# Kernel optimization log

Hardware: AMD Instinct MI355X
Metric: run time of the kernel (lower is better)

The kernel has to match this reference:

```python
import jax, jax.numpy as jnp
import numpy as np

BS, S, D, H, DFF, L = 8, 1024, 256, 8, 1024, 3
DK = D // H
NEG = -1e32


def setup_inputs() -> dict:
    key = jax.random.key(0)
    ks = jax.random.split(key, 10)
    r = lambda k, shp: jax.random.normal(k, shp, jnp.float32) * 0.02
    return {
        "q_embed_data": jax.random.normal(ks[0], (BS, S, D), jnp.float32),
        "qa_embed_data": jax.random.normal(ks[1], (BS, S, D), jnp.float32),
        "Wk": r(ks[2], (L, D, D)), "bk": jnp.zeros((L, D), jnp.float32),
        "Wv": r(ks[3], (L, D, D)), "bv": jnp.zeros((L, D), jnp.float32),
        "Wo": r(ks[4], (L, D, D)), "bo": jnp.zeros((L, D), jnp.float32),
        "gammas": r(ks[5], (L, H)),
        "ln1_g": jnp.ones((L, D), jnp.float32), "ln1_b": jnp.zeros((L, D), jnp.float32),
        "W1": r(ks[6], (L, D, DFF)), "b1": jnp.zeros((L, DFF), jnp.float32),
        "W2": r(ks[7], (L, DFF, D)), "b2": jnp.zeros((L, D), jnp.float32),
        "ln2_g": jnp.ones((L, D), jnp.float32), "ln2_b": jnp.zeros((L, D), jnp.float32),
    }


def _layernorm(x, g, b, eps=1e-5):
    mu = x.mean(-1, keepdims=True)
    var = ((x - mu) ** 2).mean(-1, keepdims=True)
    return (x - mu) * jax.lax.rsqrt(var + eps) * g + b


def _attn(xq, xk, xv, Wk, bk, Wv, bv, Wo, bo, gamma, mask, zero_pad):
    # kq_same=1: q and k both use k_linear
    bs = xq.shape[0]
    q = (xq @ Wk + bk).reshape(bs, S, H, DK).transpose(0, 2, 1, 3)  # bhsd
    k = (xk @ Wk + bk).reshape(bs, S, H, DK).transpose(0, 2, 1, 3)
    v = (xv @ Wv + bv).reshape(bs, S, H, DK).transpose(0, 2, 1, 3)
    scores = jnp.einsum('bhid,bhjd->bhij', q, k) / np.float32(np.sqrt(DK))
    mf = mask.astype(scores.dtype)
    # no-grad decay branch (detached in torch)
    p = jax.nn.softmax(jnp.where(mask, scores, NEG), axis=-1) * mf
    distcum = jnp.cumsum(p, axis=-1)
    disttot = p.sum(axis=-1, keepdims=True)
    idx = jnp.arange(S)
    pos = jnp.abs(idx[None, :] - idx[:, None]).astype(jnp.float32)[None, None]
    dist = jnp.sqrt(jnp.clip((disttot - distcum) * pos, 0.0, None))
    dist = jax.lax.stop_gradient(dist)
    g = -jax.nn.softplus(gamma)[None, :, None, None]  # (1,H,1,1)
    total_effect = jnp.clip(jnp.exp(dist * g), 1e-5, 1e5)
    scores = scores * total_effect
    attn = jax.nn.softmax(jnp.where(mask, scores, NEG), axis=-1)
    if zero_pad:
        attn = attn.at[:, :, 0, :].set(0.0)
    out = jnp.einsum('bhij,bhjd->bhid', attn, v)
    out = out.transpose(0, 2, 1, 3).reshape(bs, S, D)
    return out @ Wo + bo


def _block(i, xq, xk, xv, mask, zero_pad, apply_pos, P):
    Wk, bk, Wv, bv, Wo, bo, gam, l1g, l1b, W1, b1, W2, b2, l2g, l2b = [p[i] for p in P]
    q2 = _attn(xq, xk, xv, Wk, bk, Wv, bv, Wo, bo, gam, mask, zero_pad)
    x = _layernorm(xq + q2, l1g, l1b)
    if apply_pos:
        ff = jax.nn.relu(x @ W1 + b1) @ W2 + b2
        x = _layernorm(x + ff, l2g, l2b)
    return x


def _forward(q_embed_data, qa_embed_data, Wk, bk, Wv, bv, Wo, bo, gammas,
             ln1_g, ln1_b, W1, b1, W2, b2, ln2_g, ln2_b):
    P = (Wk, bk, Wv, bv, Wo, bo, gammas, ln1_g, ln1_b, W1, b1, W2, b2, ln2_g, ln2_b)
    tri_incl = jnp.tril(jnp.ones((S, S), bool))[None, None]       # mask=1: peek current+past
    tri_excl = jnp.tril(jnp.ones((S, S), bool), -1)[None, None]   # mask=0: strictly past
    x, y = q_embed_data, qa_embed_data
    # blocks_1 (n_blocks=1): mask=1, apply_pos=True, self-attn on y
    y = _block(0, y, y, y, tri_incl, False, True, P)
    # blocks_2 (2*n_blocks=2): alternate (mask=1, no FFN) / (mask=0, zero_pad, FFN, values=y)
    x = _block(1, x, x, x, tri_incl, False, False, P)
    x = _block(2, x, x, y, tri_excl, True, True, P)
    return x


def reference(q_embed_data, qa_embed_data, Wk, bk, Wv, bv, Wo, bo, gammas,
              ln1_g, ln1_b, W1, b1, W2, b2, ln2_g, ln2_b):
    return _forward(q_embed_data, qa_embed_data, Wk, bk, Wv, bv, Wo, bo, gammas,
                    ln1_g, ln1_b, W1, b1, W2, b2, ln2_g, ln2_b)
```

## Files before the change

### kernel.cpp

```cpp
#include <hip/hip_runtime.h>

typedef unsigned short u16;
typedef float f32x4 __attribute__((ext_vector_type(4)));
typedef __bf16 bf16x8 __attribute__((ext_vector_type(8)));
typedef u16 u16x8 __attribute__((ext_vector_type(8)));
typedef u16 u16x4 __attribute__((ext_vector_type(4)));

__device__ __forceinline__ u16 f2bf(float f) {
  union { float f; unsigned u; } v; v.f = f;
  unsigned r = (v.u + 0x7FFFu + ((v.u >> 16) & 1u)) >> 16;
  return (u16)r;
}
__device__ __forceinline__ unsigned cvtpk_bf16(float lo, float hi) {
  unsigned r;
  asm("v_cvt_pk_bf16_f32 %0, %1, %2" : "=v"(r) : "v"(lo), "v"(hi));
  return r;
}

__global__ __launch_bounds__(256) void gemm_vt_kernel(
    const u16* __restrict__ A, const u16* __restrict__ Bt,
    const float* __restrict__ bias, u16* __restrict__ vT, int M, int N, int K) {
  __shared__ u16 As[64 * 64];
  __shared__ u16 Bs[64 * 64];
  const int tid = threadIdx.x;
  const int lane = tid & 63;
  const int w = tid >> 6;
  const int m0 = blockIdx.x * 64;
  const int n0 = blockIdx.y * 64;
  const int wr = (w >> 1) * 32;
  const int wc = (w & 1) * 32;
  const int l15 = lane & 15, hi = lane >> 4;

  f32x4 acc[2][2] = {};

  for (int k0 = 0; k0 < K; k0 += 64) {
#pragma unroll
    for (int rep = 0; rep < 2; ++rep) {
      int idx = tid + rep * 256;
      int row = idx >> 3, c8 = idx & 7;
      int cs = ((c8 ^ (row & 7)) << 3);
      __builtin_amdgcn_global_load_lds(
          (const __attribute__((address_space(1))) void*)(A + (size_t)(m0 + row) * K + k0 + cs),
          (__attribute__((address_space(3))) void*)(&As[idx * 8]), 16, 0, 0);
      __builtin_amdgcn_global_load_lds(
          (const __attribute__((address_space(1))) void*)(Bt + (size_t)(n0 + row) * K + k0 + cs),
          (__attribute__((address_space(3))) void*)(&Bs[idx * 8]), 16, 0, 0);
    }
    __syncthreads();
#pragma unroll
    for (int kk = 0; kk < 2; ++kk) {
      int kb = (kk * 32 + (hi << 3)) << 1;
      bf16x8 af[2], bfr[2];
#pragma unroll
      for (int mf = 0; mf < 2; ++mf) {
        int m = wr + mf * 16 + l15;
        af[mf] = *(const bf16x8*)((const char*)As + m * 128 + (kb ^ ((m & 7) << 4)));
      }
#pragma unroll
      for (int nf = 0; nf < 2; ++nf) {
        int n = wc + nf * 16 + l15;
        bfr[nf] = *(const bf16x8*)((const char*)Bs + n * 128 + (kb ^ ((n & 7) << 4)));
      }
#pragma unroll
      for (int mf = 0; mf < 2; ++mf)
#pragma unroll
        for (int nf = 0; nf < 2; ++nf)
          acc[mf][nf] = __builtin_amdgcn_mfma_f32_16x16x32_bf16(af[mf], bfr[nf], acc[mf][nf], 0, 0, 0);
    }
    __syncthreads();
  }

#pragma unroll
  for (int mf = 0; mf < 2; ++mf)
#pragma unroll
    for (int nf = 0; nf < 2; ++nf) {
      int col = n0 + wc + nf * 16 + l15;
      float bia = bias[col];
      u16x4 tv;
#pragma unroll
      for (int r = 0; r < 4; ++r) {
        float val = acc[mf][nf][r] + bia;
        tv[r] = f2bf(val);
      }
      int row0 = m0 + wr + mf * 16 + (hi << 2);
      size_t addr = (((size_t)(row0 >> 10) * 8 + (col >> 5)) * 32 + (col & 31)) * 1024 + (row0 & 1023);
      *(u16x4*)(vT + addr) = tv;
    }
}

template <int RELU>
__global__ __launch_bounds__(256) void gemm_w_kernel(
    const u16* __restrict__ A, const u16* __restrict__ Bt,
    const float* __restrict__ bias, u16* __restrict__ Cbf,
    int M, int N, int K) {
  __shared__ u16 As[64 * 64];
  __shared__ u16 Bs[128 * 64];
  const int tid = threadIdx.x;
  const int lane = tid & 63;
  const int w = tid >> 6;
  const int m0 = blockIdx.x * 64;
  const int n0 = blockIdx.y * 128;
  const int wr = (w >> 1) * 32;
  const int wc = (w & 1) * 64;
  const int l15 = lane & 15, hi = lane >> 4;

  f32x4 acc[2][4] = {};

  for (int k0 = 0; k0 < K; k0 += 64) {
#pragma unroll
    for (int rep = 0; rep < 2; ++rep) {
      int idx = tid + rep * 256;
      int row = idx >> 3, c8 = idx & 7;
      int cs = ((c8 ^ (row & 7)) << 3);
      __builtin_amdgcn_global_load_lds(
          (const __attribute__((address_space(1))) void*)(A + (size_t)(m0 + row) * K + k0 + cs),
          (__attribute__((address_space(3))) void*)(&As[idx * 8]), 16, 0, 0);
    }
#pragma unroll
    for (int rep = 0; rep < 4; ++rep) {
      int idx = tid + rep * 256;
      int row = idx >> 3, c8 = idx & 7;
      int cs = ((c8 ^ (row & 7)) << 3);
      __builtin_amdgcn_global_load_lds(
          (const __attribute__((address_space(1))) void*)(Bt + (size_t)(n0 + row) * K + k0 + cs),
          (__attribute__((address_space(3))) void*)(&Bs[idx * 8]), 16, 0, 0);
    }
    __syncthreads();
#pragma unroll
    for (int kk = 0; kk < 2; ++kk) {
      int kb = (kk * 32 + (hi << 3)) << 1;
      bf16x8 af[2], bfr[4];
#pragma unroll
      for (int mf = 0; mf < 2; ++mf) {
        int m = wr + mf * 16 + l15;
        af[mf] = *(const bf16x8*)((const char*)As + m * 128 + (kb ^ ((m & 7) << 4)));
      }
#pragma unroll
      for (int nf = 0; nf < 4; ++nf) {
        int n = wc + nf * 16 + l15;
        bfr[nf] = *(const bf16x8*)((const char*)Bs + n * 128 + (kb ^ ((n & 7) << 4)));
      }
#pragma unroll
      for (int mf = 0; mf < 2; ++mf)
#pragma unroll
        for (int nf = 0; nf < 4; ++nf)
          acc[mf][nf] = __builtin_amdgcn_mfma_f32_16x16x32_bf16(af[mf], bfr[nf], acc[mf][nf], 0, 0, 0);
    }
    __syncthreads();
  }

#pragma unroll
  for (int mf = 0; mf < 2; ++mf)
#pragma unroll
    for (int nf = 0; nf < 4; ++nf) {
      int col = n0 + wc + nf * 16 + l15;
      float bia = bias[col];
#pragma unroll
      for (int r = 0; r < 4; ++r) {
        int row = m0 + wr + mf * 16 + (hi << 2) + r;
        float val = acc[mf][nf][r] + bia;
        if (RELU) val = fmaxf(val, 0.f);
        Cbf[(size_t)row * N + col] = f2bf(val);
      }
    }
}

__global__ __launch_bounds__(256) void gemm_kv_kernel(
    const u16* __restrict__ A, const u16* __restrict__ Bt,
    const float* __restrict__ biasK, const float* __restrict__ biasV,
    u16* __restrict__ qkbf, u16* __restrict__ vT, int M, int N, int K) {
  __shared__ u16 As[64 * 64];
  __shared__ u16 Bs[128 * 64];
  const int tid = threadIdx.x;
  const int lane = tid & 63;
  const int w = tid >> 6;
  const int m0 = blockIdx.x * 64;
  const int n0 = blockIdx.y * 128;
  const int wr = (w >> 1) * 32;
  const int wc = (w & 1) * 64;
  const int l15 = lane & 15, hi = lane >> 4;

  f32x4 acc[2][4] = {};

  for (int k0 = 0; k0 < K; k0 += 64) {
#pragma unroll
    for (int rep = 0; rep < 2; ++rep) {
      int idx = tid + rep * 256;
      int row = idx >> 3, c8 = idx & 7;
      int cs = ((c8 ^ (row & 7)) << 3);
      __builtin_amdgcn_global_load_lds(
          (const __attribute__((address_space(1))) void*)(A + (size_t)(m0 + row) * K + k0 + cs),
          (__attribute__((address_space(3))) void*)(&As[idx * 8]), 16, 0, 0);
    }
#pragma unroll
    for (int rep = 0; rep < 4; ++rep) {
      int idx = tid + rep * 256;
      int row = idx >> 3, c8 = idx & 7;
      int cs = ((c8 ^ (row & 7)) << 3);
      __builtin_amdgcn_global_load_lds(
          (const __attribute__((address_space(1))) void*)(Bt + (size_t)(n0 + row) * K + k0 + cs),
          (__attribute__((address_space(3))) void*)(&Bs[idx * 8]), 16, 0, 0);
    }
    __syncthreads();
#pragma unroll
    for (int kk = 0; kk < 2; ++kk) {
      int kb = (kk * 32 + (hi << 3)) << 1;
      bf16x8 af[2], bfr[4];
#pragma unroll
      for (int mf = 0; mf < 2; ++mf) {
        int m = wr + mf * 16 + l15;
        af[mf] = *(const bf16x8*)((const char*)As + m * 128 + (kb ^ ((m & 7) << 4)));
      }
#pragma unroll
      for (int nf = 0; nf < 4; ++nf) {
        int n = wc + nf * 16 + l15;
        bfr[nf] = *(const bf16x8*)((const char*)Bs + n * 128 + (kb ^ ((n & 7) << 4)));
      }
#pragma unroll
      for (int mf = 0; mf < 2; ++mf)
#pragma unroll
        for (int nf = 0; nf < 4; ++nf)
          acc[mf][nf] = __builtin_amdgcn_mfma_f32_16x16x32_bf16(af[mf], bfr[nf], acc[mf][nf], 0, 0, 0);
    }
    __syncthreads();
  }

#pragma unroll
  for (int mf = 0; mf < 2; ++mf)
#pragma unroll
    for (int nf = 0; nf < 4; ++nf) {
      int col = n0 + wc + nf * 16 + l15;
      const bool isV = (col >= 256);
      float bia = isV ? biasV[col - 256] : biasK[col];
      u16x4 tv;
#pragma unroll
      for (int r = 0; r < 4; ++r) {
        int row = m0 + wr + mf * 16 + (hi << 2) + r;
        float val = acc[mf][nf][r] + bia;
        if (!isV) qkbf[(size_t)row * 256 + col] = f2bf(val);
        tv[r] = f2bf(val);
      }
      if (isV) {
        int row0 = m0 + wr + mf * 16 + (hi << 2);
        int vc = col - 256;
        size_t addr = (((size_t)(row0 >> 10) * 8 + (vc >> 5)) * 32 + (vc & 31)) * 1024 + (row0 & 1023);
        *(u16x4*)(vT + addr) = tv;
      }
    }
}

__global__ __launch_bounds__(256) void gemm_ln_kernel(
    const u16* __restrict__ A, const u16* __restrict__ Bt,
    const float* __restrict__ bias, const float* __restrict__ res,
    const float* __restrict__ g, const float* __restrict__ b,
    float* __restrict__ outf, u16* __restrict__ outb, int K) {
  __shared__ u16 As[32 * 64];
  __shared__ u16 Bs[256 * 64];
  __shared__ float red[2][32][2];

  const int tid = threadIdx.x;
  const int lane = tid & 63;
  const int w = tid >> 6;
  const int rowgrp = w >> 1, colh = w & 1;
  const int m0 = blockIdx.x * 32;
  const int l15 = lane & 15, hi = lane >> 4;

  f32x4 acc[8] = {};

  for (int k0 = 0; k0 < K; k0 += 64) {
    {
      int row = tid >> 3, c8 = tid & 7;
      int cs = ((c8 ^ (row & 7)) << 3);
      __builtin_amdgcn_global_load_lds(
          (const __attribute__((address_space(1))) void*)(A + (size_t)(m0 + row) * K + k0 + cs),
          (__attribute__((address_space(3))) void*)(&As[tid * 8]), 16, 0, 0);
    }
#pragma unroll
    for (int rep = 0; rep < 8; ++rep) {
      int idx = tid + rep * 256;
      int row = idx >> 3, c8 = idx & 7;
      int cs = ((c8 ^ (row & 7)) << 3);
      __builtin_amdgcn_global_load_lds(
          (const __attribute__((address_space(1))) void*)(Bt + (size_t)row * K + k0 + cs),
          (__attribute__((address_space(3))) void*)(&Bs[idx * 8]), 16, 0, 0);
    }
    __syncthreads();
#pragma unroll
    for (int kk = 0; kk < 2; ++kk) {
      int kb = (kk * 32 + (hi << 3)) << 1;
      int m = rowgrp * 16 + l15;
      bf16x8 af = *(const bf16x8*)((const char*)As + m * 128 + (kb ^ ((m & 7) << 4)));
      bf16x8 bfr[8];
#pragma unroll
      for (int nf = 0; nf < 8; ++nf) {
        int n = colh * 128 + nf * 16 + l15;
        bfr[nf] = *(const bf16x8*)((const char*)Bs + n * 128 + (kb ^ ((n & 7) << 4)));
      }
#pragma unroll
      for (int nf = 0; nf < 8; ++nf)
        acc[nf] = __builtin_amdgcn_mfma_f32_16x16x32_bf16(af, bfr[nf], acc[nf], 0, 0, 0);
    }
    __syncthreads();
  }

  const int rbase = m0 + rowgrp * 16 + hi * 4;
  float s[4] = {0.f, 0.f, 0.f, 0.f}, ss[4] = {0.f, 0.f, 0.f, 0.f};
#pragma unroll
  for (int nf = 0; nf < 8; ++nf) {
    int col = colh * 128 + nf * 16 + l15;
    float bia = bias[col];
#pragma unroll
    for (int r = 0; r < 4; ++r) {
      float v = acc[nf][r] + bia + res[(size_t)(rbase + r) * 256 + col];
      acc[nf][r] = v;
      s[r] += v;
      ss[r] += v * v;
    }
  }
#pragma unroll
  for (int r = 0; r < 4; ++r) {
#pragma unroll
    for (int o = 1; o < 16; o <<= 1) {
      s[r] += __shfl_xor(s[r], o);
      ss[r] += __shfl_xor(ss[r], o);
    }
  }
  if (l15 == 0) {
#pragma unroll
    for (int r = 0; r < 4; ++r) {
      red[colh][rowgrp * 16 + hi * 4 + r][0] = s[r];
      red[colh][rowgrp * 16 + hi * 4 + r][1] = ss[r];
    }
  }
  __syncthreads();
  float mu[4], rs[4];
#pragma unroll
  for (int r = 0; r < 4; ++r) {
    int rr = rowgrp * 16 + hi * 4 + r;
    float S = red[0][rr][0] + red[1][rr][0];
    float SS = red[0][rr][1] + red[1][rr][1];
    mu[r] = S * (1.f / 256.f);
    float var = SS * (1.f / 256.f) - mu[r] * mu[r];
    rs[r] = rsqrtf(var + 1e-5f);
  }
#pragma unroll
  for (int nf = 0; nf < 8; ++nf) {
    int col = colh * 128 + nf * 16 + l15;
    float gv = g[col], bv = b[col];
#pragma unroll
    for (int r = 0; r < 4; ++r) {
      float o = (acc[nf][r] - mu[r]) * rs[r] * gv + bv;
      size_t addr = (size_t)(rbase + r) * 256 + col;
      outf[addr] = o;
      outb[addr] = f2bf(o);
    }
  }
}

__global__ __launch_bounds__(256) void attn_mfma_kernel(
    const u16* __restrict__ qkbf, const u16* __restrict__ vT,
    u16* __restrict__ ao, const float* __restrict__ gam, int excl) {
  __shared__ float zbuf[4][16];
  __shared__ float z2buf[4][16];
  __shared__ float accbuf[8][4][64];

  const int lane = threadIdx.x & 63, w = threadIdx.x >> 6;
  const int qt = 63 - blockIdx.y;
  const int bh = blockIdx.x;
  const int b = bh >> 3, h = bh & 7;
  const int q0 = qt * 16;
  const int l15 = lane & 15, hi = lane >> 4;
  const int i = q0 + l15;
  const float LOG2E = 1.4426950408889634f;
  const float g2 = -log1pf(__expf(gam[h])) * LOG2E;
  const float cscale = 0.17677669529663687f * LOG2E;
  const float CLIP2 = -16.609640474436812f;

  const u16* kbase = qkbf + (size_t)b * 1024 * 256 + h * 32;
  const u16* vbase = vT + (size_t)bh * 32 * 1024;
  const bf16x8 qfrag = *(const bf16x8*)(kbase + (size_t)i * 256 + hi * 8);

  const int mylim = i - excl;
  const int jmax = q0 + 15 - excl;
  const int ntiles = (jmax >> 4) + 1;
  const int C = (ntiles + 3) >> 2;
  const int c0 = w * C;
  const int tEnd = (c0 + C < ntiles) ? (c0 + C) : ntiles;
  const int count = (tEnd > c0) ? (tEnd - c0) : 0;

  auto calc_l = [&](int t, float* l) {
    bf16x8 kf = *(const bf16x8*)(kbase + (size_t)(t * 16 + l15) * 256 + hi * 8);
    f32x4 sA = {};
    sA = __builtin_amdgcn_mfma_f32_16x16x32_bf16(kf, qfrag, sA, 0, 0, 0);
    l[0] = sA[0] * cscale; l[1] = sA[1] * cscale;
    l[2] = sA[2] * cscale; l[3] = sA[3] * cscale;
    if (t == ntiles - 1) {
      const int kb = t * 16 + hi * 4;
      l[0] = (kb + 0 <= mylim) ? l[0] : -1000.f;
      l[1] = (kb + 1 <= mylim) ? l[1] : -1000.f;
      l[2] = (kb + 2 <= mylim) ? l[2] : -1000.f;
      l[3] = (kb + 3 <= mylim) ? l[3] : -1000.f;
    }
  };

  float zacc = 0.f;
  for (int t = c0; t < tEnd; ++t) {
    float l[4]; calc_l(t, l);
    zacc += (exp2f(l[0]) + exp2f(l[1])) + (exp2f(l[2]) + exp2f(l[3]));
  }
  zacc += __shfl_xor(zacc, 16);
  zacc += __shfl_xor(zacc, 32);
  if (lane < 16) zbuf[w][lane] = zacc;
  __syncthreads();

  const float zc0 = zbuf[0][l15], zc1 = zbuf[1][l15];
  const float zc2 = zbuf[2][l15], zc3 = zbuf[3][l15];
  const float Z = zc0 + zc1 + zc2 + zc3;
  const float invZ = Z > 0.f ? 1.f / Z : 0.f;
  float prefix = 0.f;
  if (w > 0) prefix += zc0;
  if (w > 1) prefix += zc1;
  if (w > 2) prefix += zc2;

  float carry = prefix, z2 = 0.f;
  f32x4 acc0 = {}, acc1 = {};

  auto sm4 = [&](const float* l, int kb) -> uint2 {
    const float e0 = exp2f(l[0]), e1 = exp2f(l[1]);
    const float e2 = exp2f(l[2]), e3 = exp2f(l[3]);
    const float cA = e0 + e1, cB2 = cA + e2, cC = cB2 + e3;
    float vsc = cC;
    float tmp = __shfl_up(vsc, 16); if (hi >= 1) vsc += tmp;
    tmp = __shfl_up(vsc, 32); if (hi >= 2) vsc += tmp;
    const float exg = vsc - cC;
    const float tot = __shfl(vsc, l15 + 48);
    const float cb = carry + exg;
    carry += tot;
    const float posb = (float)(i - kb);
    const float r0 = (Z - (cb + e0)) * invZ;
    const float r1 = (Z - (cb + cA)) * invZ;
    const float r2 = (Z - (cb + cB2)) * invZ;
    const float r3 = (Z - (cb + cC)) * invZ;
    const float d20 = fmaxf(r0 * posb, 0.f);
    const float d21 = fmaxf(r1 * (posb - 1.f), 0.f);
    const float d22 = fmaxf(r2 * (posb - 2.f), 0.f);
    const float d23 = fmaxf(r3 * (posb - 3.f), 0.f);
    const float a0 = fmaxf(__builtin_amdgcn_sqrtf(d20) * g2, CLIP2);
    const float a1 = fmaxf(__builtin_amdgcn_sqrtf(d21) * g2, CLIP2);
    const float a2 = fmaxf(__builtin_amdgcn_sqrtf(d22) * g2, CLIP2);
    const float a3 = fmaxf(__builtin_amdgcn_sqrtf(d23) * g2, CLIP2);
    const float p0 = exp2f(l[0] * exp2f(a0));
    const float p1 = exp2f(l[1] * exp2f(a1));
    const float p2 = exp2f(l[2] * exp2f(a2));
    const float p3 = exp2f(l[3] * exp2f(a3));
    z2 += (p0 + p1) + (p2 + p3);
    uint2 r; r.x = cvtpk_bf16(p0, p1); r.y = cvtpk_bf16(p2, p3);
    return r;
  };

  const int Cp = (count + 1) & ~1;
  for (int tl = 0; tl < Cp; tl += 2) {
    const int t0 = c0 + tl, t1 = t0 + 1;
    float la[4], lb[4];
    calc_l(t0, la);
    const bool v1 = (tl + 1 < count);
    if (v1) calc_l(t1, lb);
    const int jb = t0 * 16;
    bf16x8 vf0 = *(const bf16x8*)(vbase + (size_t)l15 * 1024 + jb + hi * 8);
    bf16x8 vf1 = *(const bf16x8*)(vbase + (size_t)(16 + l15) * 1024 + jb + hi * 8);
    uint2 uA = sm4(la, t0 * 16 + hi * 4);
    uint2 uB = make_uint2(0u, 0u);
    if (v1) uB = sm4(lb, t1 * 16 + hi * 4);
    const int srcA = l15 + (((2 * hi) & 3) << 4);
    const int srcB = l15 + (((2 * hi + 1) & 3) << 4);
    unsigned a00 = (unsigned)__shfl((int)uA.x, srcA);
    unsigned a01 = (unsigned)__shfl((int)uB.x, srcA);
    unsigned a10 = (unsigned)__shfl((int)uA.y, srcA);
    unsigned a11 = (unsigned)__shfl((int)uB.y, srcA);
    unsigned b00 = (unsigned)__shfl((int)uA.x, srcB);
    unsigned b01 = (unsigned)__shfl((int)uB.x, srcB);
    unsigned b10 = (unsigned)__shfl((int)uA.y, srcB);
    unsigned b11 = (unsigned)__shfl((int)uB.y, srcB);
    const bool up = hi >= 2;
    union { unsigned u[4]; bf16x8 v; } pf;
    pf.u[0] = up ? a01 : a00;
    pf.u[1] = up ? a11 : a10;
    pf.u[2] = up ? b01 : b00;
    pf.u[3] = up ? b11 : b10;
    acc0 = __builtin_amdgcn_mfma_f32_16x16x32_bf16(vf0, pf.v, acc0, 0, 0, 0);
    acc1 = __builtin_amdgcn_mfma_f32_16x16x32_bf16(vf1, pf.v, acc1, 0, 0, 0);
  }

  z2 += __shfl_xor(z2, 16);
  z2 += __shfl_xor(z2, 32);
  if (lane < 16) z2buf[w][lane] = z2;
#pragma unroll
  for (int j = 0; j < 4; ++j) {
    accbuf[j][w][lane] = acc0[j];
    accbuf[4 + j][w][lane] = acc1[j];
  }
  __syncthreads();

  if (w == 0) {
    const float z2t = z2buf[0][l15] + z2buf[1][l15] + z2buf[2][l15] + z2buf[3][l15];
    const float inv2 = z2t > 0.f ? 1.f / z2t : 0.f;
    u16* aop = ao + ((size_t)(b * 1024 + i)) * 256 + h * 32;
    float s0[4], s1[4];
#pragma unroll
    for (int j = 0; j < 4; ++j) {
      s0[j] = (accbuf[j][0][lane] + accbuf[j][1][lane] + accbuf[j][2][lane] + accbuf[j][3][lane]) * inv2;
      s1[j] = (accbuf[4 + j][0][lane] + accbuf[4 + j][1][lane] + accbuf[4 + j][2][lane] + accbuf[4 + j][3][lane]) * inv2;
    }
    uint2 o0, o1;
    o0.x = cvtpk_bf16(s0[0], s0[1]); o0.y = cvtpk_bf16(s0[2], s0[3]);
    o1.x = cvtpk_bf16(s1[0], s1[1]); o1.y = cvtpk_bf16(s1[2], s1[3]);
    *(uint2*)(aop + hi * 4) = o0;
    *(uint2*)(aop + 16 + hi * 4) = o1;
  }
}

__global__ __launch_bounds__(256) void prep_kernel(
    const float* __restrict__ Wk, const float* __restrict__ Wv,
    const float* __restrict__ Wo, const float* __restrict__ W1,
    const float* __restrict__ W2, const float* __restrict__ qe,
    const float* __restrict__ qae, u16* __restrict__ Wkvt,
    u16* __restrict__ Wot, u16* __restrict__ W1t, u16* __restrict__ W2t,
    u16* __restrict__ xbf, u16* __restrict__ ybf) {
  __shared__ float t[32][33];
  const int bid = blockIdx.x;
  const int tx = threadIdx.x, ty = threadIdx.y;

  if (bid < 2112) {
    const float* src; u16* dst;
    int K, N, n0, k0;
    size_t so, doff;
    if (bid < 576) {
      int wsel = bid / 192, r = bid % 192, z = r >> 6, tt = r & 63;
      K = 256; N = 256;
      n0 = (tt & 7) * 32; k0 = (tt >> 3) * 32;
      so = (size_t)z * 65536;
      if (wsel == 0)      { src = Wk; dst = Wkvt;        doff = (size_t)z * 131072; }
      else if (wsel == 1) { src = Wv; dst = Wkvt + 65536; doff = (size_t)z * 131072; }
      else                { src = Wo; dst = Wot;          doff = (size_t)z * 65536; }
    } else if (bid < 1344) {
      int r = bid - 576, z = r >> 8, tt = r & 255;
      K = 256; N = 1024;
      n0 = (tt & 31) * 32; k0 = (tt >> 5) * 32;
      src = W1; dst = W1t;
      so = (size_t)z * 262144; doff = (size_t)z * 262144;
    } else {
      int r = bid - 1344, z = r >> 8, tt = r & 255;
      K = 1024; N = 256;
      n0 = (tt & 7) * 32; k0 = (tt >> 3) * 32;
      src = W2; dst = W2t;
      so = (size_t)z * 262144; doff = (size_t)z * 262144;
    }
#pragma unroll
    for (int r = 0; r < 32; r += 8)
      t[ty + r][tx] = src[so + (size_t)(k0 + ty + r) * N + n0 + tx];
    __syncthreads();
#pragma unroll
    for (int r = 0; r < 32; r += 8)
      dst[doff + (size_t)(n0 + ty + r) * K + k0 + tx] = f2bf(t[tx][ty + r]);
  } else {
    int r = bid - 2112;
    const float* in = (r < 1024) ? qe : qae;
    u16* out = (r < 1024) ? xbf : ybf;
    int rr = r & 1023;
    int tid = ty * 32 + tx;
    size_t i = ((size_t)rr * 256 + tid) * 8;
    float4 a = *(const float4*)(in + i);
    float4 c = *(const float4*)(in + i + 4);
    u16x8 o;
    o[0] = f2bf(a.x); o[1] = f2bf(a.y); o[2] = f2bf(a.z); o[3] = f2bf(a.w);
    o[4] = f2bf(c.x); o[5] = f2bf(c.y); o[6] = f2bf(c.z); o[7] = f2bf(c.w);
    *(u16x8*)(out + i) = o;
  }
}

extern "C" void kernel_launch(void* const* d_in, const int* in_sizes, int n_in,
                              void* d_out, int out_size, void* d_ws,
                              size_t ws_size, hipStream_t stream) {
  const float* q_embed = (const float*)d_in[0];
  const float* qa_embed = (const float*)d_in[1];
  const float* Wk = (const float*)d_in[2];
  const float* bk = (const float*)d_in[3];
  const float* Wv = (const float*)d_in[4];
  const float* bv = (const float*)d_in[5];
  const float* Wo = (const float*)d_in[6];
  const float* bo = (const float*)d_in[7];
  const float* gammas = (const float*)d_in[8];
  const float* ln1_g = (const float*)d_in[9];
  const float* ln1_b = (const float*)d_in[10];
  const float* W1 = (const float*)d_in[11];
  const float* b1 = (const float*)d_in[12];
  const float* W2 = (const float*)d_in[13];
  const float* b2 = (const float*)d_in[14];
  const float* ln2_g = (const float*)d_in[15];
  const float* ln2_b = (const float*)d_in[16];

  const size_t ACT_F32 = (size_t)8192 * 256 * 4;
  const size_t ACT_BF = (size_t)8192 * 256 * 2;
  char* p = (char*)d_ws;
  auto carve = [&](size_t bytes) {
    void* r = (void*)p;
    p += (bytes + 255) & ~(size_t)255;
    return r;
  };
  float* yb = (float*)carve(ACT_F32);
  float* xb = (float*)carve(ACT_F32);
  u16* xbf = (u16*)carve(ACT_BF);
  u16* ybf = (u16*)carve(ACT_BF);
  u16* qkbf = (u16*)carve(ACT_BF);
  u16* vTb = (u16*)carve(ACT_BF);
  u16* aobf = (u16*)carve(ACT_BF);
  u16* hbf = (u16*)carve((size_t)8192 * 1024 * 2);
  u16* Wkvt = (u16*)carve((size_t)3 * 131072 * 2);
  u16* Wot = (u16*)carve((size_t)3 * 65536 * 2);
  u16* W1t = (u16*)carve((size_t)3 * 262144 * 2);
  u16* W2t = (u16*)carve((size_t)3 * 262144 * 2);

  prep_kernel<<<4160, dim3(32, 8), 0, stream>>>(
      Wk, Wv, Wo, W1, W2, q_embed, qa_embed, Wkvt, Wot, W1t, W2t, xbf, ybf);

  const dim3 gKV(128, 4), gW1(128, 8), gVT(128, 4);
  const dim3 gA(64, 64);

  gemm_kv_kernel<<<gKV, 256, 0, stream>>>(ybf, Wkvt, bk, bv, qkbf, vTb, 8192, 512, 256);
  attn_mfma_kernel<<<gA, 256, 0, stream>>>(qkbf, vTb, aobf, gammas, 0);
  gemm_ln_kernel<<<256, 256, 0, stream>>>(aobf, Wot, bo, qa_embed, ln1_g, ln1_b, yb, ybf, 256);
  gemm_w_kernel<1><<<gW1, 256, 0, stream>>>(ybf, W1t, b1, hbf, 8192, 1024, 256);
  gemm_ln_kernel<<<256, 256, 0, stream>>>(hbf, W2t, b2, yb, ln2_g, ln2_b, yb, ybf, 1024);

  gemm_kv_kernel<<<gKV, 256, 0, stream>>>(xbf, Wkvt + 131072, bk + 256, bv + 256, qkbf, vTb, 8192, 512, 256);
  attn_mfma_kernel<<<gA, 256, 0, stream>>>(qkbf, vTb, aobf, gammas + 8, 0);
  gemm_ln_kernel<<<256, 256, 0, stream>>>(aobf, Wot + 65536, bo + 256, q_embed, ln1_g + 256, ln1_b + 256, xb, xbf, 256);

  gemm_kv_kernel<<<gKV, 256, 0, stream>>>(xbf, Wkvt + 262144, bk + 512, bv + 512, qkbf, vTb, 8192, 512, 256);
  gemm_vt_kernel<<<gVT, 256, 0, stream>>>(ybf, Wkvt + 262144 + 65536, bv + 512, vTb, 8192, 256, 256);
  attn_mfma_kernel<<<gA, 256, 0, stream>>>(qkbf, vTb, aobf, gammas + 16, 1);
  gemm_ln_kernel<<<256, 256, 0, stream>>>(aobf, Wot + 131072, bo + 512, xb, ln1_g + 512, ln1_b + 512, xb, xbf, 256);
  gemm_w_kernel<1><<<gW1, 256, 0, stream>>>(xbf, W1t + 524288, b1 + 2048, hbf, 8192, 1024, 256);
  gemm_ln_kernel<<<256, 256, 0, stream>>>(hbf, W2t + 524288, b2 + 512, xb, ln2_g + 512, ln2_b + 512, (float*)d_out, xbf, 1024);
}
```

Baseline: 307.5 us.

## Batch independent layer-0 and layer-1 attention stages into shared launches via grid z

Layer 0 (on y) and layer 1 (on x) are independent, so their KV projection, attention and output-projection+LN kernels now run as single launches with a grid z/y dimension picking the layer. Each layer gets its own qk, vT and attention-output buffers. This removes three launches and doubles the grid per launch, so the GPU is better filled and kernel tails overlap. The cost is more workspace memory and a reordered schedule, where layer 0's FFN now runs after layer 1's attention.

```diff
diff --git a/kernel.cpp b/kernel.cpp
--- a/kernel.cpp
+++ b/kernel.cpp
@@ -5,6 +5,8 @@
 typedef __bf16 bf16x8 __attribute__((ext_vector_type(8)));
 typedef u16 u16x8 __attribute__((ext_vector_type(8)));
 typedef u16 u16x4 __attribute__((ext_vector_type(4)));
+
+#define LAYER_STRIDE 2097152
 
 __device__ __forceinline__ u16 f2bf(float f) {
   union { float f; unsigned u; } v; v.f = f;
@@ -166,11 +168,21 @@
 }
 
 __global__ __launch_bounds__(256) void gemm_kv_kernel(
-    const u16* __restrict__ A, const u16* __restrict__ Bt,
-    const float* __restrict__ biasK, const float* __restrict__ biasV,
-    u16* __restrict__ qkbf, u16* __restrict__ vT, int M, int N, int K) {
+    const u16* __restrict__ A0, const u16* __restrict__ A1,
+    const u16* __restrict__ WkvtBase, const float* __restrict__ bkBase,
+    const float* __restrict__ bvBase, u16* __restrict__ qk2,
+    u16* __restrict__ vT2) {
   __shared__ u16 As[64 * 64];
   __shared__ u16 Bs[128 * 64];
+  const int z = blockIdx.z;
+  const u16* A = z ? A1 : A0;
+  const u16* Bt = WkvtBase + (size_t)z * 131072;
+  const float* biasK = bkBase + z * 256;
+  const float* biasV = bvBase + z * 256;
+  u16* qkbf = qk2 + (size_t)z * LAYER_STRIDE;
+  u16* vT = vT2 + (size_t)z * LAYER_STRIDE;
+  const int K = 256;
+
   const int tid = threadIdx.x;
   const int lane = tid & 63;
   const int w = tid >> 6;
@@ -250,13 +262,25 @@
 }
 
 __global__ __launch_bounds__(256) void gemm_ln_kernel(
-    const u16* __restrict__ A, const u16* __restrict__ Bt,
-    const float* __restrict__ bias, const float* __restrict__ res,
-    const float* __restrict__ g, const float* __restrict__ b,
-    float* __restrict__ outf, u16* __restrict__ outb, int K) {
+    const u16* __restrict__ Abase, const u16* __restrict__ BtBase,
+    const float* __restrict__ biasBase, const float* __restrict__ res0,
+    const float* __restrict__ res1, const float* __restrict__ gBase,
+    const float* __restrict__ bBase, float* __restrict__ outf0,
+    float* __restrict__ outf1, u16* __restrict__ outb0,
+    u16* __restrict__ outb1, int K) {
   __shared__ u16 As[32 * 64];
   __shared__ u16 Bs[256 * 64];
   __shared__ float red[2][32][2];
+
+  const int z = blockIdx.y;
+  const u16* A = Abase + (size_t)z * LAYER_STRIDE;
+  const u16* Bt = BtBase + (size_t)z * 65536;
+  const float* bias = biasBase + z * 256;
+  const float* res = z ? res1 : res0;
+  const float* g = gBase + z * 256;
+  const float* b = bBase + z * 256;
+  float* outf = z ? outf1 : outf0;
+  u16* outb = z ? outb1 : outb0;
 
   const int tid = threadIdx.x;
   const int lane = tid & 63;
@@ -358,11 +382,17 @@
 }
 
 __global__ __launch_bounds__(256) void attn_mfma_kernel(
-    const u16* __restrict__ qkbf, const u16* __restrict__ vT,
-    u16* __restrict__ ao, const float* __restrict__ gam, int excl) {
+    const u16* __restrict__ qk2, const u16* __restrict__ vT2,
+    u16* __restrict__ ao2, const float* __restrict__ gamBase, int excl) {
   __shared__ float zbuf[4][16];
   __shared__ float z2buf[4][16];
   __shared__ float accbuf[8][4][64];
+
+  const int z = blockIdx.z;
+  const u16* qkbf = qk2 + (size_t)z * LAYER_STRIDE;
+  const u16* vT = vT2 + (size_t)z * LAYER_STRIDE;
+  u16* ao = ao2 + (size_t)z * LAYER_STRIDE;
+  const float* gam = gamBase + z * 8;
 
   const int lane = threadIdx.x & 63, w = threadIdx.x >> 6;
   const int qt = 63 - blockIdx.y;
@@ -611,9 +641,9 @@
   float* xb = (float*)carve(ACT_F32);
   u16* xbf = (u16*)carve(ACT_BF);
   u16* ybf = (u16*)carve(ACT_BF);
-  u16* qkbf = (u16*)carve(ACT_BF);
-  u16* vTb = (u16*)carve(ACT_BF);
-  u16* aobf = (u16*)carve(ACT_BF);
+  u16* qk2 = (u16*)carve(2 * ACT_BF);
+  u16* vT2 = (u16*)carve(2 * ACT_BF);
+  u16* ao2 = (u16*)carve(2 * ACT_BF);
   u16* hbf = (u16*)carve((size_t)8192 * 1024 * 2);
   u16* Wkvt = (u16*)carve((size_t)3 * 131072 * 2);
   u16* Wot = (u16*)carve((size_t)3 * 65536 * 2);
@@ -623,23 +653,20 @@
   prep_kernel<<<4160, dim3(32, 8), 0, stream>>>(
       Wk, Wv, Wo, W1, W2, q_embed, qa_embed, Wkvt, Wot, W1t, W2t, xbf, ybf);
 
-  const dim3 gKV(128, 4), gW1(128, 8), gVT(128, 4);
-  const dim3 gA(64, 64);
-
-  gemm_kv_kernel<<<gKV, 256, 0, stream>>>(ybf, Wkvt, bk, bv, qkbf, vTb, 8192, 512, 256);
-  attn_mfma_kernel<<<gA, 256, 0, stream>>>(qkbf, vTb, aobf, gammas, 0);
-  gemm_ln_kernel<<<256, 256, 0, stream>>>(aobf, Wot, bo, qa_embed, ln1_g, ln1_b, yb, ybf, 256);
-  gemm_w_kernel<1><<<gW1, 256, 0, stream>>>(ybf, W1t, b1, hbf, 8192, 1024, 256);
-  gemm_ln_kernel<<<256, 256, 0, stream>>>(hbf, W2t, b2, yb, ln2_g, ln2_b, yb, ybf, 1024);
-
-  gemm_kv_kernel<<<gKV, 256, 0, stream>>>(xbf, Wkvt + 131072, bk + 256, bv + 256, qkbf, vTb, 8192, 512, 256);
-  attn_mfma_kernel<<<gA, 256, 0, stream>>>(qkbf, vTb, aobf, gammas + 8, 0);
-  gemm_ln_kernel<<<256, 256, 0, stream>>>(aobf, Wot + 65536, bo + 256, q_embed, ln1_g + 256, ln1_b + 256, xb, xbf, 256);
-
-  gemm_kv_kernel<<<gKV, 256, 0, stream>>>(xbf, Wkvt + 262144, bk + 512, bv + 512, qkbf, vTb, 8192, 512, 256);
-  gemm_vt_kernel<<<gVT, 256, 0, stream>>>(ybf, Wkvt + 262144 + 65536, bv + 512, vTb, 8192, 256, 256);
-  attn_mfma_kernel<<<gA, 256, 0, stream>>>(qkbf, vTb, aobf, gammas + 16, 1);
-  gemm_ln_kernel<<<256, 256, 0, stream>>>(aobf, Wot + 131072, bo + 512, xb, ln1_g + 512, ln1_b + 512, xb, xbf, 256);
-  gemm_w_kernel<1><<<gW1, 256, 0, stream>>>(xbf, W1t + 524288, b1 + 2048, hbf, 8192, 1024, 256);
-  gemm_ln_kernel<<<256, 256, 0, stream>>>(hbf, W2t + 524288, b2 + 512, xb, ln2_g + 512, ln2_b + 512, (float*)d_out, xbf, 1024);
-}
+  gemm_kv_kernel<<<dim3(128, 4, 2), 256, 0, stream>>>(ybf, xbf, Wkvt, bk, bv, qk2, vT2);
+  attn_mfma_kernel<<<dim3(64, 64, 2), 256, 0, stream>>>(qk2, vT2, ao2, gammas, 0);
+  gemm_ln_kernel<<<dim3(256, 2), 256, 0, stream>>>(
+      ao2, Wot, bo, qa_embed, q_embed, ln1_g, ln1_b, yb, xb, ybf, xbf, 256);
+  gemm_w_kernel<1><<<dim3(128, 8), 256, 0, stream>>>(ybf, W1t, b1, hbf, 8192, 1024, 256);
+  gemm_ln_kernel<<<dim3(256, 1), 256, 0, stream>>>(
+      hbf, W2t, b2, yb, yb, ln2_g, ln2_b, yb, yb, ybf, ybf, 1024);
+
+  gemm_kv_kernel<<<dim3(128, 4, 1), 256, 0, stream>>>(xbf, xbf, Wkvt + 262144, bk + 512, bv + 512, qk2, vT2);
+  gemm_vt_kernel<<<dim3(128, 4), 256, 0, stream>>>(ybf, Wkvt + 262144 + 65536, bv + 512, vT2, 8192, 256, 256);
+  attn_mfma_kernel<<<dim3(64, 64, 1), 256, 0, stream>>>(qk2, vT2, ao2, gammas + 16, 1);
+  gemm_ln_kernel<<<dim3(256, 1), 256, 0, stream>>>(
+      ao2, Wot + 131072, bo + 512, xb, xb, ln1_g + 512, ln1_b + 512, xb, xb, xbf, xbf, 256);
+  gemm_w_kernel<1><<<dim3(128, 8), 256, 0, stream>>>(xbf, W1t + 524288, b1 + 2048, hbf, 8192, 1024, 256);
+  gemm_ln_kernel<<<dim3(256, 1), 256, 0, stream>>>(
+      hbf, W2t + 524288, b2 + 512, xb, xb, ln2_g + 512, ln2_b + 512, (float*)d_out, (float*)d_out, xbf, xbf, 1024);
+}
```

Result: faster. 290.5 us (-5.5%).
